# Performance work log

Hardware: AMD Instinct MI355X
Metric: run time of the kernel (lower is better)

## Reference

```python
import jax, jax.numpy as jnp
import numpy as np

NF, NH1, NH21, NH22, NCLS = 6, 128, 128, 128, 3
OBS_X, OBS_Y, OBS_Z, R = 10.0, 10.0, 9.0, 7.0
BATCH = 131072


def setup_inputs() -> dict:
    key = jax.random.key(0)
    ks = jax.random.split(key, 16)
    def lin(kw, kb, fan_in, fan_out):
        bound = 1.0 / np.sqrt(fan_in)
        w = jax.random.uniform(kw, (fan_out, fan_in), jnp.float32, -bound, bound)
        b = jax.random.uniform(kb, (fan_out,), jnp.float32, -bound, bound)
        return w, b
    fc1_w, fc1_b = lin(ks[0], ks[1], NF, NH1)
    fc21_w, fc21_b = lin(ks[2], ks[3], NH1, NH21)
    fc22_w, fc22_b = lin(ks[4], ks[5], NH1, NH22)
    fcm1_w, fcm1_b = lin(ks[6], ks[7], NH21, NH21)
    fcm2_w, fcm2_b = lin(ks[8], ks[9], NH22, NH22)
    fc31_w, fc31_b = lin(ks[10], ks[11], NH21, NCLS)
    fc32_w, fc32_b = lin(ks[12], ks[13], NH22, 2)
    x = jax.random.normal(ks[14], (BATCH, NF), jnp.float32)
    mean = jnp.array([10.0, 0.0, 10.0, 0.0, 9.0, 0.0], jnp.float32)
    std = jnp.array([5.0, 2.0, 5.0, 2.0, 5.0, 2.0], jnp.float32)
    return {"x": x, "mean": mean, "std": std,
            "fc1_w": fc1_w, "fc1_b": fc1_b,
            "fc21_w": fc21_w, "fc21_b": fc21_b,
            "fc22_w": fc22_w, "fc22_b": fc22_b,
            "fcm1_w": fcm1_w, "fcm1_b": fcm1_b,
            "fcm2_w": fcm2_w, "fcm2_b": fcm2_b,
            "fc31_w": fc31_w, "fc31_b": fc31_b,
            "fc32_w": fc32_w, "fc32_b": fc32_b,
            "sgn": 1}


def _forward(x, mean, std, fc1_w, fc1_b, fc21_w, fc21_b, fc22_w, fc22_b,
             fcm1_w, fcm1_b, fcm2_w, fcm2_b, fc31_w, fc31_b, fc32_w, fc32_b):
    x0 = x * std + mean                                   # de-normalized state [B,6]
    h = jnp.tanh(x @ fc1_w.T + fc1_b)                     # [B,NH1]
    x21 = jnp.tanh(h @ fc21_w.T + fc21_b)
    x22 = jnp.tanh(h @ fc22_w.T + fc22_b)
    x21 = jnp.tanh(x21 @ fcm1_w.T + fcm1_b)
    x22 = jnp.tanh(x22 @ fcm2_w.T + fcm2_b)
    x31 = x21 @ fc31_w.T + fc31_b                         # QP linear term p, [B,3]
    x32 = 4.0 * jax.nn.sigmoid(x22 @ fc32_w.T + fc32_b)   # HOCBF penalties, [B,2]

    # higher-order CBF terms
    px, vx, py, vy, pz, vz = (x0[:, i] for i in range(6))
    dx, dy, dz = px - OBS_X, py - OBS_Y, pz - OBS_Z
    barrier = dx**4 + dy**4 + dz**4 - R**4
    barrier_dot = 4.0 * (dx**3 * vx + dy**3 * vy + dz**3 * vz)
    Lf2b = 12.0 * (dx**2 * vx**2 + dy**2 * vy**2 + dz**2 * vz**2)
    G = -4.0 * jnp.stack([dx**3, dy**3, dz**3], axis=-1)  # [B,3], single constraint G u <= h
    hvec = Lf2b + (x32[:, 0] + x32[:, 1]) * barrier_dot + x32[:, 0] * x32[:, 1] * barrier  # [B]

    # QP: min 0.5 u^T u + x31^T u  s.t.  G u <= h  (Q = I, one constraint)
    # Closed-form KKT: u = -x31 - lam*G, lam = max(0, (G @ (-x31) - h) / (G @ G))
    u_unc = -x31
    Gu = jnp.sum(G * u_unc, axis=-1)                      # [B]
    GG = jnp.sum(G * G, axis=-1)                          # [B]
    lam = jnp.maximum(Gu - hvec, 0.0) / GG
    u = u_unc - lam[:, None] * G                          # [B,3]
    return u


def reference(x, mean, std, fc1_w, fc1_b, fc21_w, fc21_b, fc22_w, fc22_b,
              fcm1_w, fcm1_b, fcm2_w, fcm2_b, fc31_w, fc31_b, fc32_w, fc32_b, sgn):
    return _forward(x, mean, std, fc1_w, fc1_b, fc21_w, fc21_b, fc22_w, fc22_b,
                    fcm1_w, fcm1_b, fcm2_w, fcm2_b, fc31_w, fc31_b, fc32_w, fc32_b)
```

## Files before the change

kernel.cpp:

```cpp
#include <hip/hip_runtime.h>

typedef _Float16 half8 __attribute__((ext_vector_type(8)));
typedef _Float16 half4_t __attribute__((ext_vector_type(4)));
typedef __fp16 fp16x2 __attribute__((ext_vector_type(2)));
typedef float float4_t __attribute__((ext_vector_type(4)));
typedef float float2_t __attribute__((ext_vector_type(2)));

#define SB 32
#define NT 512
#define RS (SB * 8)

#define OFF_W1   0
#define OFF_W21  4096
#define OFF_W22  20480
#define OFF_WM1  36864
#define OFF_WM2  53248
#define OFF_W4A  69632
#define OFF_BIAS 73728
#define WS_HELEMS 73728

#define SCL_TANH 2.8853900817779268f
#define SCL_SIG  -1.4426950408889634f

__device__ __forceinline__ float tanh_pre(float a) {
  float e = __builtin_amdgcn_exp2f(a);
  return fmaf(-2.f, __builtin_amdgcn_rcpf(1.f + e), 1.f);
}
__device__ __forceinline__ half4_t pack4(float v0, float v1, float v2, float v3) {
  fp16x2 lo = __builtin_amdgcn_cvt_pkrtz(v0, v1);
  fp16x2 hi = __builtin_amdgcn_cvt_pkrtz(v2, v3);
  half4_t h;
  h[0] = (_Float16)lo[0]; h[1] = (_Float16)lo[1];
  h[2] = (_Float16)hi[0]; h[3] = (_Float16)hi[1];
  return h;
}

__global__ void prepack(const float* __restrict__ w1, const float* __restrict__ w21,
                        const float* __restrict__ w22, const float* __restrict__ wm1,
                        const float* __restrict__ wm2, const float* __restrict__ w31,
                        const float* __restrict__ w32, const float* __restrict__ b1,
                        const float* __restrict__ b21, const float* __restrict__ b22,
                        const float* __restrict__ bm1, const float* __restrict__ bm2,
                        _Float16* __restrict__ ws) {
  const int stride = gridDim.x * blockDim.x;
  for (int i = blockIdx.x * blockDim.x + threadIdx.x; i < WS_HELEMS; i += stride) {
    float v;
    if (i < OFF_W21) {
      int t = i;
      int j = t & 7, c = t >> 3, l16 = c & 15, t1 = c >> 4;
      int k8 = t1 & 3, mt = t1 >> 2;
      int row = mt * 16 + l16, k = k8 * 8 + j;
      v = (k < 6) ? w1[row * 6 + k] * SCL_TANH : 0.f;
    } else if (i < OFF_W4A) {
      int t = i - OFF_W21;
      int m = t >> 14; t &= 16383;
      const float* src = (m == 0) ? w21 : (m == 1) ? w22 : (m == 2) ? wm1 : wm2;
      int j = t & 7, c = t >> 3, l16 = c & 15, t1 = c >> 4;
      int k8 = t1 & 15, mt = t1 >> 4;
      v = src[(mt * 16 + l16) * 128 + k8 * 8 + j] * SCL_TANH;
    } else {
      int t = i - OFF_W4A;
      int j = t & 7, r = t >> 3, l16 = r & 15, q = r >> 4;
      int cc = q & 15, chain = q >> 4;
      int k = cc * 8 + j, m = l16;
      if (chain == 0) v = (m < 3) ? w31[m * 128 + k] : 0.f;
      else            v = (m < 2) ? w32[m * 128 + k] * SCL_SIG : 0.f;
    }
    ws[i] = (_Float16)v;
  }
  float* bws = (float*)(ws + OFF_BIAS);
  for (int i = blockIdx.x * blockDim.x + threadIdx.x; i < 640; i += stride) {
    int layer = i >> 7, idx = i & 127;
    const float* src = (layer == 0) ? b1 : (layer == 1) ? b21
                     : (layer == 2) ? b22 : (layer == 3) ? bm1 : bm2;
    bws[i] = src[idx] * SCL_TANH;
  }
}

__device__ __forceinline__ void layer128(const half8* __restrict__ A, float4_t bv,
                                         const _Float16* __restrict__ inB,
                                         _Float16* __restrict__ outB,
                                         int quad, int l16, int wv) {
  float4_t acc[2];
  acc[0] = bv; acc[1] = bv;
#pragma unroll
  for (int kk = 0; kk < 4; ++kk) {
#pragma unroll
    for (int nt = 0; nt < 2; ++nt) {
      half8 b = *(const half8*)(inB + (kk * 4 + quad) * RS + (nt * 16 + l16) * 8);
      acc[nt] = __builtin_amdgcn_mfma_f32_16x16x32_f16(A[kk], b, acc[nt], 0, 0, 0);
    }
  }
  const int ob = wv * 16 + quad * 4;
  _Float16* base = outB + (ob >> 3) * RS + (ob & 7);
#pragma unroll
  for (int nt = 0; nt < 2; ++nt) {
    const int s = nt * 16 + l16;
    half4_t h = pack4(tanh_pre(acc[nt][0]), tanh_pre(acc[nt][1]),
                      tanh_pre(acc[nt][2]), tanh_pre(acc[nt][3]));
    *(half4_t*)(base + s * 8) = h;
  }
}

__global__ __launch_bounds__(NT, 6) void bnet_main(
    const float* __restrict__ x, const float* __restrict__ meang,
    const float* __restrict__ stdg, const float* __restrict__ b31,
    const float* __restrict__ b32, const _Float16* __restrict__ ws,
    float* __restrict__ out) {
  __shared__ __align__(16) _Float16 bufH[SB * 128];
  __shared__ __align__(16) _Float16 bufA[SB * 128];
  __shared__ __align__(16) _Float16 bufB[SB * 128];
  __shared__ __align__(16) _Float16 bufC[SB * 128];

  const int tid = threadIdx.x;
  const int wv = tid >> 6;
  const int lane = tid & 63;
  const int quad = lane >> 4;
  const int l16 = lane & 15;
  const int s0 = blockIdx.x * SB;
  const float* biasF = (const float*)(ws + OFF_BIAS);
  const int arow = (wv * 16 + quad * 4);

  half8 A1 = *(const half8*)(ws + OFF_W1 + ((wv * 4 + quad) * 16 + l16) * 8);
  float4_t bv1 = *(const float4_t*)(biasF + arow);
  float4_t bv21 = *(const float4_t*)(biasF + 128 + arow);
  float4_t bv22 = *(const float4_t*)(biasF + 256 + arow);
  float4_t bvm1 = *(const float4_t*)(biasF + 384 + arow);
  float4_t bvm2 = *(const float4_t*)(biasF + 512 + arow);
  half8 A21[4];
#pragma unroll
  for (int kk = 0; kk < 4; ++kk)
    A21[kk] = *(const half8*)(ws + OFF_W21 + ((wv * 16 + kk * 4 + quad) * 16 + l16) * 8);

  {
    float4_t acc[2];
    acc[0] = bv1; acc[1] = bv1;
#pragma unroll
    for (int nt = 0; nt < 2; ++nt) {
      half8 v;
#pragma unroll
      for (int j = 0; j < 8; ++j) v[j] = (_Float16)0.f;
      if (quad == 0) {
        const float* xp = x + (size_t)(s0 + nt * 16 + l16) * 6;
        float2_t e0 = *(const float2_t*)(xp);
        float2_t e1 = *(const float2_t*)(xp + 2);
        float2_t e2 = *(const float2_t*)(xp + 4);
        v[0] = (_Float16)e0[0]; v[1] = (_Float16)e0[1];
        v[2] = (_Float16)e1[0]; v[3] = (_Float16)e1[1];
        v[4] = (_Float16)e2[0]; v[5] = (_Float16)e2[1];
      }
      acc[nt] = __builtin_amdgcn_mfma_f32_16x16x32_f16(A1, v, acc[nt], 0, 0, 0);
    }
    _Float16* base = bufH + (arow >> 3) * RS + (arow & 7);
#pragma unroll
    for (int nt = 0; nt < 2; ++nt) {
      const int s = nt * 16 + l16;
      half4_t h = pack4(tanh_pre(acc[nt][0]), tanh_pre(acc[nt][1]),
                        tanh_pre(acc[nt][2]), tanh_pre(acc[nt][3]));
      *(half4_t*)(base + s * 8) = h;
    }
  }
  half8 A22[4];
#pragma unroll
  for (int kk = 0; kk < 4; ++kk)
    A22[kk] = *(const half8*)(ws + OFF_W22 + ((wv * 16 + kk * 4 + quad) * 16 + l16) * 8);
  __syncthreads();

  layer128(A21, bv21, bufH, bufA, quad, l16, wv);
  half8 AM1[4];
#pragma unroll
  for (int kk = 0; kk < 4; ++kk)
    AM1[kk] = *(const half8*)(ws + OFF_WM1 + ((wv * 16 + kk * 4 + quad) * 16 + l16) * 8);
  layer128(A22, bv22, bufH, bufB, quad, l16, wv);
  __syncthreads();

  half8 AM2[4];
#pragma unroll
  for (int kk = 0; kk < 4; ++kk)
    AM2[kk] = *(const half8*)(ws + OFF_WM2 + ((wv * 16 + kk * 4 + quad) * 16 + l16) * 8);
  layer128(AM1, bvm1, bufA, bufH, quad, l16, wv);
  layer128(AM2, bvm2, bufB, bufC, quad, l16, wv);
  __syncthreads();

  if (wv == 0) {
    half8 A4[2][4];
#pragma unroll
    for (int c = 0; c < 2; ++c)
#pragma unroll
      for (int kk = 0; kk < 4; ++kk)
        A4[c][kk] = *(const half8*)(ws + OFF_W4A +
                                    ((c * 16 + kk * 4 + quad) * 16 + l16) * 8);
    float4_t a0[2], a1[2];
#pragma unroll
    for (int nt = 0; nt < 2; ++nt) {
      a0[nt] = (float4_t){0.f, 0.f, 0.f, 0.f};
      a1[nt] = (float4_t){0.f, 0.f, 0.f, 0.f};
      if (quad == 0) {
        a0[nt][0] = b31[0]; a0[nt][1] = b31[1]; a0[nt][2] = b31[2];
        a1[nt][0] = b32[0] * SCL_SIG; a1[nt][1] = b32[1] * SCL_SIG;
      }
    }
#pragma unroll
    for (int kk = 0; kk < 4; ++kk)
#pragma unroll
      for (int nt = 0; nt < 2; ++nt) {
        half8 bh = *(const half8*)(bufH + (kk * 4 + quad) * RS + (nt * 16 + l16) * 8);
        half8 bc = *(const half8*)(bufC + (kk * 4 + quad) * RS + (nt * 16 + l16) * 8);
        a0[nt] = __builtin_amdgcn_mfma_f32_16x16x32_f16(A4[0][kk], bh, a0[nt], 0, 0, 0);
        a1[nt] = __builtin_amdgcn_mfma_f32_16x16x32_f16(A4[1][kk], bc, a1[nt], 0, 0, 0);
      }
    if (quad == 0) {
      const float m0 = meang[0], m1 = meang[1], m2 = meang[2];
      const float m3 = meang[3], m4 = meang[4], m5 = meang[5];
      const float sd0 = stdg[0], sd1 = stdg[1], sd2 = stdg[2];
      const float sd3 = stdg[3], sd4 = stdg[4], sd5 = stdg[5];
#pragma unroll
      for (int nt = 0; nt < 2; ++nt) {
        const int s = nt * 16 + l16;
        float u0 = -a0[nt][0];
        float u1 = -a0[nt][1];
        float u2 = -a0[nt][2];
        float p0 = 4.f * __builtin_amdgcn_rcpf(1.f + __builtin_amdgcn_exp2f(a1[nt][0]));
        float p1 = 4.f * __builtin_amdgcn_rcpf(1.f + __builtin_amdgcn_exp2f(a1[nt][1]));
        const float* xp = x + (size_t)(s0 + s) * 6;
        float2_t e0 = *(const float2_t*)(xp);
        float2_t e1 = *(const float2_t*)(xp + 2);
        float2_t e2 = *(const float2_t*)(xp + 4);
        float px = e0[0] * sd0 + m0, vx = e0[1] * sd1 + m1;
        float py = e1[0] * sd2 + m2, vy = e1[1] * sd3 + m3;
        float pz = e2[0] * sd4 + m4, vz = e2[1] * sd5 + m5;
        float dx = px - 10.f, dy = py - 10.f, dz = pz - 9.f;
        float dx2 = dx * dx, dy2 = dy * dy, dz2 = dz * dz;
        float dx3 = dx2 * dx, dy3 = dy2 * dy, dz3 = dz2 * dz;
        float barrier = dx3 * dx + dy3 * dy + dz3 * dz - 2401.f;
        float bdot = 4.f * (dx3 * vx + dy3 * vy + dz3 * vz);
        float Lf2b = 12.f * (dx2 * vx * vx + dy2 * vy * vy + dz2 * vz * vz);
        float g0 = -4.f * dx3, g1 = -4.f * dy3, g2 = -4.f * dz3;
        float hv = Lf2b + (p0 + p1) * bdot + p0 * p1 * barrier;
        float Gu = g0 * u0 + g1 * u1 + g2 * u2;
        float GG = g0 * g0 + g1 * g1 + g2 * g2;
        float lam = fmaxf(Gu - hv, 0.f) / GG;
        float* op = out + (size_t)(s0 + s) * 3;
        op[0] = u0 - lam * g0;
        op[1] = u1 - lam * g1;
        op[2] = u2 - lam * g2;
      }
    }
  }
}

extern "C" void kernel_launch(void* const* d_in, const int* in_sizes, int n_in,
                              void* d_out, int out_size, void* d_ws, size_t ws_size,
                              hipStream_t stream) {
  const float* x    = (const float*)d_in[0];
  const float* mean = (const float*)d_in[1];
  const float* stdv = (const float*)d_in[2];
  const float* w1   = (const float*)d_in[3];
  const float* b1   = (const float*)d_in[4];
  const float* w21  = (const float*)d_in[5];
  const float* b21  = (const float*)d_in[6];
  const float* w22  = (const float*)d_in[7];
  const float* b22  = (const float*)d_in[8];
  const float* wm1  = (const float*)d_in[9];
  const float* bm1  = (const float*)d_in[10];
  const float* wm2  = (const float*)d_in[11];
  const float* bm2  = (const float*)d_in[12];
  const float* w31  = (const float*)d_in[13];
  const float* b31  = (const float*)d_in[14];
  const float* w32  = (const float*)d_in[15];
  const float* b32  = (const float*)d_in[16];
  _Float16* ws = (_Float16*)d_ws;
  float* out = (float*)d_out;
  const int batch = in_sizes[0] / 6;

  hipLaunchKernelGGL(prepack, dim3(96), dim3(256), 0, stream,
                     w1, w21, w22, wm1, wm2, w31, w32,
                     b1, b21, b22, bm1, bm2, ws);
  hipLaunchKernelGGL(bnet_main, dim3(batch / SB), dim3(NT), 0, stream,
                     x, mean, stdv, b31, b32, (const _Float16*)ws, out);
}
```

Measured before the change: 126.4 us.

## Double per-block sample tile and split output head across four waves

```diff
diff --git a/kernel.cpp b/kernel.cpp
--- a/kernel.cpp
+++ b/kernel.cpp
@@ -6,7 +6,7 @@
 typedef float float4_t __attribute__((ext_vector_type(4)));
 typedef float float2_t __attribute__((ext_vector_type(2)));
 
-#define SB 32
+#define SB 64
 #define NT 512
 #define RS (SB * 8)
 
@@ -81,12 +81,12 @@
                                          const _Float16* __restrict__ inB,
                                          _Float16* __restrict__ outB,
                                          int quad, int l16, int wv) {
-  float4_t acc[2];
-  acc[0] = bv; acc[1] = bv;
+  float4_t acc[4];
+  acc[0] = bv; acc[1] = bv; acc[2] = bv; acc[3] = bv;
 #pragma unroll
   for (int kk = 0; kk < 4; ++kk) {
 #pragma unroll
-    for (int nt = 0; nt < 2; ++nt) {
+    for (int nt = 0; nt < 4; ++nt) {
       half8 b = *(const half8*)(inB + (kk * 4 + quad) * RS + (nt * 16 + l16) * 8);
       acc[nt] = __builtin_amdgcn_mfma_f32_16x16x32_f16(A[kk], b, acc[nt], 0, 0, 0);
     }
@@ -94,7 +94,7 @@
   const int ob = wv * 16 + quad * 4;
   _Float16* base = outB + (ob >> 3) * RS + (ob & 7);
 #pragma unroll
-  for (int nt = 0; nt < 2; ++nt) {
+  for (int nt = 0; nt < 4; ++nt) {
     const int s = nt * 16 + l16;
     half4_t h = pack4(tanh_pre(acc[nt][0]), tanh_pre(acc[nt][1]),
                       tanh_pre(acc[nt][2]), tanh_pre(acc[nt][3]));
@@ -102,7 +102,7 @@
   }
 }
 
-__global__ __launch_bounds__(NT, 6) void bnet_main(
+__global__ __launch_bounds__(NT, 4) void bnet_main(
     const float* __restrict__ x, const float* __restrict__ meang,
     const float* __restrict__ stdg, const float* __restrict__ b31,
     const float* __restrict__ b32, const _Float16* __restrict__ ws,
@@ -133,10 +133,10 @@
     A21[kk] = *(const half8*)(ws + OFF_W21 + ((wv * 16 + kk * 4 + quad) * 16 + l16) * 8);
 
   {
-    float4_t acc[2];
-    acc[0] = bv1; acc[1] = bv1;
-#pragma unroll
-    for (int nt = 0; nt < 2; ++nt) {
+    float4_t acc[4];
+    acc[0] = bv1; acc[1] = bv1; acc[2] = bv1; acc[3] = bv1;
+#pragma unroll
+    for (int nt = 0; nt < 4; ++nt) {
       half8 v;
 #pragma unroll
       for (int j = 0; j < 8; ++j) v[j] = (_Float16)0.f;
@@ -153,7 +153,7 @@
     }
     _Float16* base = bufH + (arow >> 3) * RS + (arow & 7);
 #pragma unroll
-    for (int nt = 0; nt < 2; ++nt) {
+    for (int nt = 0; nt < 4; ++nt) {
       const int s = nt * 16 + l16;
       half4_t h = pack4(tanh_pre(acc[nt][0]), tanh_pre(acc[nt][1]),
                         tanh_pre(acc[nt][2]), tanh_pre(acc[nt][3]));
@@ -172,79 +172,73 @@
   for (int kk = 0; kk < 4; ++kk)
     AM1[kk] = *(const half8*)(ws + OFF_WM1 + ((wv * 16 + kk * 4 + quad) * 16 + l16) * 8);
   layer128(A22, bv22, bufH, bufB, quad, l16, wv);
+  half8 AM2[4];
+#pragma unroll
+  for (int kk = 0; kk < 4; ++kk)
+    AM2[kk] = *(const half8*)(ws + OFF_WM2 + ((wv * 16 + kk * 4 + quad) * 16 + l16) * 8);
   __syncthreads();
 
-  half8 AM2[4];
-#pragma unroll
-  for (int kk = 0; kk < 4; ++kk)
-    AM2[kk] = *(const half8*)(ws + OFF_WM2 + ((wv * 16 + kk * 4 + quad) * 16 + l16) * 8);
-  layer128(AM1, bvm1, bufA, bufH, quad, l16, wv);
-  layer128(AM2, bvm2, bufB, bufC, quad, l16, wv);
-  __syncthreads();
-
-  if (wv == 0) {
-    half8 A4[2][4];
+  layer128(AM1, bvm1, bufA, bufC, quad, l16, wv);
+  half8 A4[2][4];
+  if (wv < 4) {
 #pragma unroll
     for (int c = 0; c < 2; ++c)
 #pragma unroll
       for (int kk = 0; kk < 4; ++kk)
         A4[c][kk] = *(const half8*)(ws + OFF_W4A +
                                     ((c * 16 + kk * 4 + quad) * 16 + l16) * 8);
-    float4_t a0[2], a1[2];
-#pragma unroll
-    for (int nt = 0; nt < 2; ++nt) {
-      a0[nt] = (float4_t){0.f, 0.f, 0.f, 0.f};
-      a1[nt] = (float4_t){0.f, 0.f, 0.f, 0.f};
-      if (quad == 0) {
-        a0[nt][0] = b31[0]; a0[nt][1] = b31[1]; a0[nt][2] = b31[2];
-        a1[nt][0] = b32[0] * SCL_SIG; a1[nt][1] = b32[1] * SCL_SIG;
-      }
-    }
-#pragma unroll
-    for (int kk = 0; kk < 4; ++kk)
-#pragma unroll
-      for (int nt = 0; nt < 2; ++nt) {
-        half8 bh = *(const half8*)(bufH + (kk * 4 + quad) * RS + (nt * 16 + l16) * 8);
-        half8 bc = *(const half8*)(bufC + (kk * 4 + quad) * RS + (nt * 16 + l16) * 8);
-        a0[nt] = __builtin_amdgcn_mfma_f32_16x16x32_f16(A4[0][kk], bh, a0[nt], 0, 0, 0);
-        a1[nt] = __builtin_amdgcn_mfma_f32_16x16x32_f16(A4[1][kk], bc, a1[nt], 0, 0, 0);
-      }
+  }
+  layer128(AM2, bvm2, bufB, bufH, quad, l16, wv);
+  __syncthreads();
+
+  if (wv < 4) {
+    const int nt = wv;
+    float4_t c0 = (float4_t){0.f, 0.f, 0.f, 0.f};
+    float4_t c1 = (float4_t){0.f, 0.f, 0.f, 0.f};
     if (quad == 0) {
+      c0[0] = b31[0]; c0[1] = b31[1]; c0[2] = b31[2];
+      c1[0] = b32[0] * SCL_SIG; c1[1] = b32[1] * SCL_SIG;
+    }
+#pragma unroll
+    for (int kk = 0; kk < 4; ++kk) {
+      half8 bh = *(const half8*)(bufC + (kk * 4 + quad) * RS + (nt * 16 + l16) * 8);
+      half8 bc = *(const half8*)(bufH + (kk * 4 + quad) * RS + (nt * 16 + l16) * 8);
+      c0 = __builtin_amdgcn_mfma_f32_16x16x32_f16(A4[0][kk], bh, c0, 0, 0, 0);
+      c1 = __builtin_amdgcn_mfma_f32_16x16x32_f16(A4[1][kk], bc, c1, 0, 0, 0);
+    }
+    if (quad == 0) {
+      const int s = nt * 16 + l16;
+      float u0 = -c0[0];
+      float u1 = -c0[1];
+      float u2 = -c0[2];
+      float p0 = 4.f * __builtin_amdgcn_rcpf(1.f + __builtin_amdgcn_exp2f(c1[0]));
+      float p1 = 4.f * __builtin_amdgcn_rcpf(1.f + __builtin_amdgcn_exp2f(c1[1]));
       const float m0 = meang[0], m1 = meang[1], m2 = meang[2];
       const float m3 = meang[3], m4 = meang[4], m5 = meang[5];
       const float sd0 = stdg[0], sd1 = stdg[1], sd2 = stdg[2];
       const float sd3 = stdg[3], sd4 = stdg[4], sd5 = stdg[5];
-#pragma unroll
-      for (int nt = 0; nt < 2; ++nt) {
-        const int s = nt * 16 + l16;
-        float u0 = -a0[nt][0];
-        float u1 = -a0[nt][1];
-        float u2 = -a0[nt][2];
-        float p0 = 4.f * __builtin_amdgcn_rcpf(1.f + __builtin_amdgcn_exp2f(a1[nt][0]));
-        float p1 = 4.f * __builtin_amdgcn_rcpf(1.f + __builtin_amdgcn_exp2f(a1[nt][1]));
-        const float* xp = x + (size_t)(s0 + s) * 6;
-        float2_t e0 = *(const float2_t*)(xp);
-        float2_t e1 = *(const float2_t*)(xp + 2);
-        float2_t e2 = *(const float2_t*)(xp + 4);
-        float px = e0[0] * sd0 + m0, vx = e0[1] * sd1 + m1;
-        float py = e1[0] * sd2 + m2, vy = e1[1] * sd3 + m3;
-        float pz = e2[0] * sd4 + m4, vz = e2[1] * sd5 + m5;
-        float dx = px - 10.f, dy = py - 10.f, dz = pz - 9.f;
-        float dx2 = dx * dx, dy2 = dy * dy, dz2 = dz * dz;
-        float dx3 = dx2 * dx, dy3 = dy2 * dy, dz3 = dz2 * dz;
-        float barrier = dx3 * dx + dy3 * dy + dz3 * dz - 2401.f;
-        float bdot = 4.f * (dx3 * vx + dy3 * vy + dz3 * vz);
-        float Lf2b = 12.f * (dx2 * vx * vx + dy2 * vy * vy + dz2 * vz * vz);
-        float g0 = -4.f * dx3, g1 = -4.f * dy3, g2 = -4.f * dz3;
-        float hv = Lf2b + (p0 + p1) * bdot + p0 * p1 * barrier;
-        float Gu = g0 * u0 + g1 * u1 + g2 * u2;
-        float GG = g0 * g0 + g1 * g1 + g2 * g2;
-        float lam = fmaxf(Gu - hv, 0.f) / GG;
-        float* op = out + (size_t)(s0 + s) * 3;
-        op[0] = u0 - lam * g0;
-        op[1] = u1 - lam * g1;
-        op[2] = u2 - lam * g2;
-      }
+      const float* xp = x + (size_t)(s0 + s) * 6;
+      float2_t e0 = *(const float2_t*)(xp);
+      float2_t e1 = *(const float2_t*)(xp + 2);
+      float2_t e2 = *(const float2_t*)(xp + 4);
+      float px = e0[0] * sd0 + m0, vx = e0[1] * sd1 + m1;
+      float py = e1[0] * sd2 + m2, vy = e1[1] * sd3 + m3;
+      float pz = e2[0] * sd4 + m4, vz = e2[1] * sd5 + m5;
+      float dx = px - 10.f, dy = py - 10.f, dz = pz - 9.f;
+      float dx2 = dx * dx, dy2 = dy * dy, dz2 = dz * dz;
+      float dx3 = dx2 * dx, dy3 = dy2 * dy, dz3 = dz2 * dz;
+      float barrier = dx3 * dx + dy3 * dy + dz3 * dz - 2401.f;
+      float bdot = 4.f * (dx3 * vx + dy3 * vy + dz3 * vz);
+      float Lf2b = 12.f * (dx2 * vx * vx + dy2 * vy * vy + dz2 * vz * vz);
+      float g0 = -4.f * dx3, g1 = -4.f * dy3, g2 = -4.f * dz3;
+      float hv = Lf2b + (p0 + p1) * bdot + p0 * p1 * barrier;
+      float Gu = g0 * u0 + g1 * u1 + g2 * u2;
+      float GG = g0 * g0 + g1 * g1 + g2 * g2;
+      float lam = fmaxf(Gu - hv, 0.f) / GG;
+      float* op = out + (size_t)(s0 + s) * 3;
+      op[0] = u0 - lam * g0;
+      op[1] = u1 - lam * g1;
+      op[2] = u2 - lam * g2;
     }
   }
 }
```

New measurement: 120.8 us. 1.05x faster.
